# Kernel tuning notes

Measured on AMD Instinct MI355X. Metric: run time of the kernel, lower is better.

Reference implementation:

```python
import jax, jax.numpy as jnp
import numpy as np

B, N, E, H, AD, V, STEPS = 32, 256, 4, 512, 256, 10000, 5


def setup_inputs() -> dict:
    key = jax.random.key(0)
    ks = jax.random.split(key, 16)
    s = 0.02  # xavier-ish init scale
    return {
        "annotation": jax.random.randint(ks[0], (B, N), 0, V),
        "A": jax.random.normal(ks[1], (B, N, 2 * N * E), dtype=jnp.float32),
        "emb": jax.random.normal(ks[2], (V, AD), dtype=jnp.float32) * s,
        "W_in": jax.random.normal(ks[3], (E, H, H), dtype=jnp.float32) * s,
        "b_in": jnp.zeros((E, H), jnp.float32),
        "W_out": jax.random.normal(ks[4], (E, H, H), dtype=jnp.float32) * s,
        "b_out": jnp.zeros((E, H), jnp.float32),
        "Wr": jax.random.normal(ks[5], (3 * H, H), dtype=jnp.float32) * s,
        "br": jnp.zeros((H,), jnp.float32),
        "Wz": jax.random.normal(ks[6], (3 * H, H), dtype=jnp.float32) * s,
        "bz": jnp.zeros((H,), jnp.float32),
        "Wh": jax.random.normal(ks[7], (3 * H, H), dtype=jnp.float32) * s,
        "bh": jnp.zeros((H,), jnp.float32),
        "Wo": jax.random.normal(ks[8], (H + AD, H), dtype=jnp.float32) * s,
        "bo": jnp.zeros((H,), jnp.float32),
    }


def reference(annotation, A, emb, W_in, b_in, W_out, b_out,
              Wr, br, Wz, bz, Wh, bh, Wo, bo):
    ann = emb[annotation]                                   # [B, N, AD]
    pad = jnp.zeros((B, N, H - AD), ann.dtype)
    prop = jnp.concatenate([ann, pad], axis=2)              # [B, N, H]
    A_in, A_out = A[:, :, :N * E], A[:, :, N * E:]          # [B, N, N*E] each

    for _ in range(STEPS):
        # fused per-edge-type linears: [B, E, N, H] -> [B, E*N, H]
        ins = (jnp.einsum('bnd,edh->benh', prop, W_in)
               + b_in[None, :, None, :]).reshape(B, E * N, H)
        outs = (jnp.einsum('bnd,edh->benh', prop, W_out)
                + b_out[None, :, None, :]).reshape(B, E * N, H)
        a_in = jnp.matmul(A_in, ins)                        # [B, N, H]
        a_out = jnp.matmul(A_out, outs)                     # [B, N, H]
        a = jnp.concatenate([a_in, a_out, prop], axis=2)    # [B, N, 3H]
        r = jax.nn.sigmoid(a @ Wr + br)
        z = jax.nn.sigmoid(a @ Wz + bz)
        j = jnp.concatenate([a_in, a_out, r * prop], axis=2)
        h_hat = jnp.tanh(j @ Wh + bh)
        prop = (1.0 - z) * prop + z * h_hat

    join = jnp.concatenate([prop, ann], axis=2)             # [B, N, H+AD]
    return jnp.tanh(join @ Wo + bo)                         # [B, N, H]
```

## Files before the change

kernel.cpp:

```cpp
#include <hip/hip_runtime.h>
#include <hip/hip_bf16.h>
#include <cstdint>
#include <cstddef>

typedef unsigned short u16;
typedef _Float16 f16;
typedef f16 f16x8 __attribute__((ext_vector_type(8)));
typedef float f32x4 __attribute__((ext_vector_type(4)));

static __device__ inline u16 f2h(float f) {
    f16 h = (f16)f;
    return *reinterpret_cast<u16*>(&h);
}
static __device__ inline float h2f(u16 u) {
    f16 h = *reinterpret_cast<f16*>(&u);
    return (float)h;
}

#define GLL(g, l) __builtin_amdgcn_global_load_lds(                    \
    (const __attribute__((address_space(1))) void*)(g),                \
    (__attribute__((address_space(3))) void*)(l), 16, 0, 0)

static __device__ inline int xcd_swz(int fid, int nwg) {
    const int q = nwg >> 3;
    return (fid & 7) * q + (fid >> 3);
}

static __device__ inline void stage_tile(const u16* __restrict__ src, int ld,
                                         u16* lds, int wave, int lane) {
    const int r = lane >> 2;
    const int c = (lane & 3) << 3;
    const u16* g0 = src + (size_t)(wave * 32 + r) * ld + c;
    GLL(g0, lds + wave * 1024);
    GLL(g0 + (size_t)16 * ld, lds + wave * 1024 + 512);
}

static __device__ inline void compute32(const u16* lA, const u16* lB,
                                        int wq_r, int wq_c, int lr, int lk,
                                        f32x4 acc[4][4]) {
    f16x8 a[4], b[4];
    #pragma unroll
    for (int i = 0; i < 4; ++i)
        a[i] = *reinterpret_cast<const f16x8*>(&lA[(wq_r + i * 16 + lr) * 32 + lk]);
    #pragma unroll
    for (int j = 0; j < 4; ++j)
        b[j] = *reinterpret_cast<const f16x8*>(&lB[(wq_c + j * 16 + lr) * 32 + lk]);
    #pragma unroll
    for (int i = 0; i < 4; ++i)
        #pragma unroll
        for (int j = 0; j < 4; ++j)
            acc[i][j] = __builtin_amdgcn_mfma_f32_16x16x32_f16(a[i], b[j], acc[i][j], 0, 0, 0);
}

static __device__ inline void gemm128(const u16* __restrict__ a1, int lda1, int ka1,
                                      const u16* __restrict__ a2, int lda2,
                                      const u16* __restrict__ bt, int ldb,
                                      int K, int m0, int n0,
                                      u16* sA, u16* sB, f32x4 acc[4][4])
{
    const int t = threadIdx.x, lane = t & 63, wave = t >> 6;
    const int lr = lane & 15, lk = (lane >> 4) << 3;
    const int wq_r = (wave >> 1) << 6, wq_c = (wave & 1) << 6;
    const int nt = K >> 5;
    stage_tile(a1 + (size_t)m0 * lda1, lda1, sA, wave, lane);
    stage_tile(bt + (size_t)n0 * ldb, ldb, sB, wave, lane);
    __syncthreads();
    int buf = 0;
    for (int ti = 0; ti < nt; ++ti) {
        const int k1 = (ti + 1) << 5;
        if (k1 < K) {
            const u16* s;
            int ld;
            if (k1 < ka1) { s = a1 + (size_t)m0 * lda1 + k1;        ld = lda1; }
            else          { s = a2 + (size_t)m0 * lda2 + (k1 - ka1); ld = lda2; }
            stage_tile(s, ld, sA + (buf ^ 1) * 4096, wave, lane);
            stage_tile(bt + (size_t)n0 * ldb + k1, ldb, sB + (buf ^ 1) * 4096, wave, lane);
        }
        compute32(sA + buf * 4096, sB + buf * 4096, wq_r, wq_c, lr, lk, acc);
        __syncthreads();
        buf ^= 1;
    }
}

#define EPI                                         \
    const int lane = threadIdx.x & 63;              \
    const int wave = threadIdx.x >> 6;              \
    const int wq_r = (wave >> 1) << 6;              \
    const int wq_c = (wave & 1) << 6;               \
    const int lr = lane & 15;                       \
    const int l4 = (lane >> 4) << 2;

#define TDIR (32ull * 512 * 1024)

__global__ __launch_bounds__(256, 4) void k_proj(const u16* __restrict__ P,
                                                 const u16* __restrict__ Wio,
                                                 const float* __restrict__ b_in,
                                                 const float* __restrict__ b_out,
                                                 u16* __restrict__ T)
{
    __shared__ u16 sA[2 * 4096], sB[2 * 4096];
    const int fid = xcd_swz(blockIdx.x, gridDim.x);
    const int n = fid & 31, m = fid >> 5;
    const int m0 = m << 7, n0 = n << 7;
    f32x4 acc[4][4] = {};
    gemm128(P, 512, 512, P, 512, Wio, 512, 512, m0, n0, sA, sB, acc);
    EPI
    #pragma unroll
    for (int i = 0; i < 4; ++i) {
        const int row = m0 + wq_r + i * 16 + l4;
        const int b = row >> 8, mm = row & 255;
        #pragma unroll
        for (int j = 0; j < 4; ++j) {
            const int col = n0 + wq_c + j * 16 + lr;
            const int dir = col >> 11, eh = col & 2047;
            const float bia = (dir ? b_out : b_in)[eh];
            const int e = eh >> 9, h = eh & 511;
            ushort4 w4;
            w4.x = f2h(acc[i][j][0] + bia);
            w4.y = f2h(acc[i][j][1] + bia);
            w4.z = f2h(acc[i][j][2] + bia);
            w4.w = f2h(acc[i][j][3] + bia);
            u16* dst = T + (size_t)dir * TDIR + (size_t)b * 512 * 1024 + (size_t)h * 1024 + e * 256 + mm;
            *reinterpret_cast<ushort4*>(dst) = w4;
        }
    }
}

__global__ __launch_bounds__(256, 4) void k_amat(const u16* __restrict__ A16,
                                                 const u16* __restrict__ T,
                                                 u16* __restrict__ acat)
{
    __shared__ u16 sA[2 * 4096], sB[2 * 4096];
    const int fid = xcd_swz(blockIdx.x, gridDim.x);
    const int n = fid & 3, m = (fid >> 2) & 1, bd = fid >> 3;
    const int b = bd >> 1, dir = bd & 1;
    const int m0 = m << 7, n0 = n << 7;
    const u16* A1 = A16 + (size_t)b * 256 * 2048 + dir * 1024;
    const u16* Bt = T + (size_t)dir * TDIR + (size_t)b * 512 * 1024;
    f32x4 acc[4][4] = {};
    gemm128(A1, 2048, 1024, A1, 2048, Bt, 1024, 1024, m0, n0, sA, sB, acc);
    EPI
    #pragma unroll
    for (int i = 0; i < 4; ++i) {
        const int row = m0 + wq_r + i * 16 + l4;
        #pragma unroll
        for (int j = 0; j < 4; ++j) {
            const int col = n0 + wq_c + j * 16 + lr;
            #pragma unroll
            for (int v = 0; v < 4; ++v)
                acat[((size_t)b * 256 + row + v) * 1024 + dir * 512 + col] = f2h(acc[i][j][v]);
        }
    }
}

__global__ __launch_bounds__(256, 4) void k_gates(const u16* __restrict__ acat,
                                                  const u16* __restrict__ P,
                                                  const u16* __restrict__ Wrzh,
                                                  const float* __restrict__ br,
                                                  const float* __restrict__ bz,
                                                  u16* __restrict__ rp,
                                                  float* __restrict__ z,
                                                  float* __restrict__ hpart)
{
    __shared__ u16 sA[2 * 4096], sB[2 * 4096];
    const int fid = xcd_swz(blockIdx.x, gridDim.x);
    const int n = fid % 12, m = fid / 12;
    const int m0 = m << 7, n0 = n << 7;
    f32x4 acc[4][4] = {};
    gemm128(acat, 1024, 1024, P, 512, Wrzh, 1536, 1536, m0, n0, sA, sB, acc);
    EPI
    #pragma unroll
    for (int i = 0; i < 4; ++i) {
        const int row = m0 + wq_r + i * 16 + l4;
        #pragma unroll
        for (int j = 0; j < 4; ++j) {
            const int col = n0 + wq_c + j * 16 + lr;
            if (col < 512) {
                const float bia = br[col];
                #pragma unroll
                for (int v = 0; v < 4; ++v) {
                    const float s = 1.0f / (1.0f + __expf(-(acc[i][j][v] + bia)));
                    const size_t idx = (size_t)(row + v) * 512 + col;
                    rp[idx] = f2h(s * h2f(P[idx]));
                }
            } else if (col < 1024) {
                const float bia = bz[col - 512];
                #pragma unroll
                for (int v = 0; v < 4; ++v)
                    z[(size_t)(row + v) * 512 + (col - 512)] =
                        1.0f / (1.0f + __expf(-(acc[i][j][v] + bia)));
            } else {
                #pragma unroll
                for (int v = 0; v < 4; ++v)
                    hpart[(size_t)(row + v) * 512 + (col - 1024)] = acc[i][j][v];
            }
        }
    }
}

__global__ __launch_bounds__(256, 4) void k_hup(const u16* __restrict__ rp,
                                                const u16* __restrict__ WhP,
                                                const float* __restrict__ bh,
                                                const float* __restrict__ z,
                                                const float* __restrict__ hpart,
                                                u16* __restrict__ P)
{
    __shared__ u16 sA[2 * 4096], sB[2 * 4096];
    const int fid = xcd_swz(blockIdx.x, gridDim.x);
    const int n = fid & 3, m = fid >> 2;
    const int m0 = m << 7, n0 = n << 7;
    f32x4 acc[4][4] = {};
    gemm128(rp, 512, 512, rp, 512, WhP, 512, 512, m0, n0, sA, sB, acc);
    EPI
    #pragma unroll
    for (int i = 0; i < 4; ++i) {
        const int row = m0 + wq_r + i * 16 + l4;
        #pragma unroll
        for (int j = 0; j < 4; ++j) {
            const int col = n0 + wq_c + j * 16 + lr;
            const float bia = bh[col];
            #pragma unroll
            for (int v = 0; v < 4; ++v) {
                const size_t idx = (size_t)(row + v) * 512 + col;
                const float hh = tanhf(hpart[idx] + acc[i][j][v] + bia);
                const float zz = z[idx];
                const float pn = (1.0f - zz) * h2f(P[idx]) + zz * hh;
                P[idx] = f2h(pn);
            }
        }
    }
}

__global__ __launch_bounds__(256, 4) void k_final(const u16* __restrict__ P,
                                                  const u16* __restrict__ annf,
                                                  const u16* __restrict__ Wj,
                                                  const float* __restrict__ bo,
                                                  float* __restrict__ out)
{
    __shared__ u16 sA[2 * 4096], sB[2 * 4096];
    const int fid = xcd_swz(blockIdx.x, gridDim.x);
    const int n = fid & 3, m = fid >> 2;
    const int m0 = m << 7, n0 = n << 7;
    f32x4 acc[4][4] = {};
    gemm128(P, 512, 512, annf, 256, Wj, 768, 768, m0, n0, sA, sB, acc);
    EPI
    #pragma unroll
    for (int i = 0; i < 4; ++i) {
        const int row = m0 + wq_r + i * 16 + l4;
        #pragma unroll
        for (int j = 0; j < 4; ++j) {
            const int col = n0 + wq_c + j * 16 + lr;
            const float bia = bo[col];
            #pragma unroll
            for (int v = 0; v < 4; ++v)
                out[(size_t)(row + v) * 512 + col] = tanhf(acc[i][j][v] + bia);
        }
    }
}

__global__ void s_gather(const int* __restrict__ ann, const float* __restrict__ emb,
                         u16* __restrict__ P, u16* __restrict__ annf)
{
    const int gid = blockIdx.x * 256 + threadIdx.x;
    const int row = gid >> 9, d = gid & 511;
    float v = 0.0f;
    if (d < 256) v = emb[(size_t)ann[row] * 256 + d];
    const u16 h = f2h(v);
    P[gid] = h;
    if (d < 256) annf[((size_t)row << 8) + d] = h;
}

__global__ void s_cvtA(const float* __restrict__ src, u16* __restrict__ dst)
{
    const size_t base = ((size_t)blockIdx.x * 256 + threadIdx.x) * 8;
    float4 f0 = *reinterpret_cast<const float4*>(src + base);
    float4 f1 = *reinterpret_cast<const float4*>(src + base + 4);
    ushort4 p0 = { f2h(f0.x), f2h(f0.y), f2h(f0.z), f2h(f0.w) };
    ushort4 p1 = { f2h(f1.x), f2h(f1.y), f2h(f1.z), f2h(f1.w) };
    *reinterpret_cast<ushort4*>(dst + base)     = p0;
    *reinterpret_cast<ushort4*>(dst + base + 4) = p1;
}

__global__ void s_wio(const float* __restrict__ Wi, const float* __restrict__ Wo,
                      u16* __restrict__ dst)
{
    const int gid = blockIdx.x * 256 + threadIdx.x;
    if (gid >= 4096 * 512) return;
    const int nn = gid >> 9, k = gid & 511;
    const int dir = nn >> 11, e = (nn >> 9) & 3, h = nn & 511;
    const float* W = dir ? Wo : Wi;
    dst[gid] = f2h(W[(size_t)e * 512 * 512 + (size_t)k * 512 + h]);
}

__global__ void s_wrzh(const float* __restrict__ Wr, const float* __restrict__ Wz,
                       const float* __restrict__ Wh, u16* __restrict__ dst)
{
    const int gid = blockIdx.x * 256 + threadIdx.x;
    if (gid >= 1536 * 1536) return;
    const int nn = gid / 1536, k = gid - nn * 1536;
    float v;
    if (nn < 512)       v = Wr[(size_t)k * 512 + nn];
    else if (nn < 1024) v = Wz[(size_t)k * 512 + (nn - 512)];
    else                v = (k < 1024) ? Wh[(size_t)k * 512 + (nn - 1024)] : 0.0f;
    dst[gid] = f2h(v);
}

__global__ void s_whp(const float* __restrict__ Wh, u16* __restrict__ dst)
{
    const int gid = blockIdx.x * 256 + threadIdx.x;
    if (gid >= 512 * 512) return;
    const int nn = gid >> 9, k = gid & 511;
    dst[gid] = f2h(Wh[(size_t)(1024 + k) * 512 + nn]);
}

__global__ void s_wj(const float* __restrict__ Wo, u16* __restrict__ dst)
{
    const int gid = blockIdx.x * 256 + threadIdx.x;
    if (gid >= 512 * 768) return;
    const int nn = gid / 768, k = gid - nn * 768;
    dst[gid] = f2h(Wo[(size_t)k * 512 + nn]);
}

extern "C" void kernel_launch(void* const* d_in, const int* in_sizes, int n_in,
                              void* d_out, int out_size, void* d_ws, size_t ws_size,
                              hipStream_t stream) {
    const int*   ann   = (const int*)d_in[0];
    const float* A     = (const float*)d_in[1];
    const float* emb   = (const float*)d_in[2];
    const float* W_in  = (const float*)d_in[3];
    const float* b_in  = (const float*)d_in[4];
    const float* W_out = (const float*)d_in[5];
    const float* b_out = (const float*)d_in[6];
    const float* Wr    = (const float*)d_in[7];
    const float* br    = (const float*)d_in[8];
    const float* Wz    = (const float*)d_in[9];
    const float* bz    = (const float*)d_in[10];
    const float* Wh    = (const float*)d_in[11];
    const float* bh    = (const float*)d_in[12];
    const float* Wo    = (const float*)d_in[13];
    const float* bo    = (const float*)d_in[14];
    float* out = (float*)d_out;

    char* ws = (char*)d_ws;
    size_t off = 0;
    auto alloc = [&](size_t bytes) -> void* {
        void* p = ws + off;
        off = (off + bytes + 255) & ~(size_t)255;
        return p;
    };
    float* z_f32 = (float*)alloc(8192ull * 512 * 4);
    float* hpart = (float*)alloc(8192ull * 512 * 4);
    u16* P     = (u16*)alloc(8192ull * 512 * 2);
    u16* rp    = (u16*)alloc(8192ull * 512 * 2);
    u16* annf  = (u16*)alloc(8192ull * 256 * 2);
    u16* acat  = (u16*)alloc(8192ull * 1024 * 2);
    u16* A16   = (u16*)alloc(8192ull * 2048 * 2);
    u16* T     = (u16*)alloc(2 * TDIR * 2);
    u16* WioT  = (u16*)alloc(4096ull * 512 * 2);
    u16* WrzhT = (u16*)alloc(1536ull * 1536 * 2);
    u16* WhPT  = (u16*)alloc(512ull * 512 * 2);
    u16* WjT   = (u16*)alloc(512ull * 768 * 2);

    s_gather<<<16384, 256, 0, stream>>>(ann, emb, P, annf);
    s_cvtA<<<8192, 256, 0, stream>>>(A, A16);
    s_wio<<<(4096 * 512 + 255) / 256, 256, 0, stream>>>(W_in, W_out, WioT);
    s_wrzh<<<(1536 * 1536 + 255) / 256, 256, 0, stream>>>(Wr, Wz, Wh, WrzhT);
    s_whp<<<(512 * 512 + 255) / 256, 256, 0, stream>>>(Wh, WhPT);
    s_wj<<<(512 * 768 + 255) / 256, 256, 0, stream>>>(Wo, WjT);

    for (int s = 0; s < 5; ++s) {
        k_proj<<<2048, 256, 0, stream>>>(P, WioT, b_in, b_out, T);
        k_amat<<<512, 256, 0, stream>>>(A16, T, acat);
        k_gates<<<768, 256, 0, stream>>>(acat, P, WrzhT, br, bz, rp, z_f32, hpart);
        k_hup<<<256, 256, 0, stream>>>(rp, WhPT, bh, z_f32, hpart, P);
    }
    k_final<<<256, 256, 0, stream>>>(P, annf, WjT, bo, out);
}
```

Baseline: 965.4 us.

## Replace 128x128 GEMM tiles with 256x256 eight-wave pipelined GEMM for three kernels

Adds a gemm256 routine that uses 512-thread blocks, 256x256 output tiles and 64-wide K slices. It stages A/B halves into XOR-swizzled LDS with global_load_lds and runs a phased schedule that interleaves loads with MFMA bursts, using explicit vmcnt waits, barriers and setprio. k_proj, k_amat and k_gates move to this routine with smaller grids, which should raise data reuse per block and cut LDS bank conflicts. The cost is far fewer blocks: k_amat drops to 128 blocks, which can underfill the 256 CUs, and the hand-written wait counts are fragile.

```diff
diff --git a/kernel.cpp b/kernel.cpp
--- a/kernel.cpp
+++ b/kernel.cpp
@@ -8,11 +8,11 @@
 typedef f16 f16x8 __attribute__((ext_vector_type(8)));
 typedef float f32x4 __attribute__((ext_vector_type(4)));
 
-static __device__ inline u16 f2h(float f) {
+static __device__ __forceinline__ u16 f2h(float f) {
     f16 h = (f16)f;
     return *reinterpret_cast<u16*>(&h);
 }
-static __device__ inline float h2f(u16 u) {
+static __device__ __forceinline__ float h2f(u16 u) {
     f16 h = *reinterpret_cast<f16*>(&u);
     return (float)h;
 }
@@ -21,13 +21,237 @@
     (const __attribute__((address_space(1))) void*)(g),                \
     (__attribute__((address_space(3))) void*)(l), 16, 0, 0)
 
-static __device__ inline int xcd_swz(int fid, int nwg) {
+#define BARR() __builtin_amdgcn_s_barrier()
+#define VMCNT(n) { asm volatile("s_waitcnt vmcnt(" #n ")" ::: "memory"); \
+                   __builtin_amdgcn_sched_barrier(0); }
+
+static __device__ __forceinline__ int xcd_swz(int fid, int nwg) {
     const int q = nwg >> 3;
     return (fid & 7) * q + (fid >> 3);
 }
 
-static __device__ inline void stage_tile(const u16* __restrict__ src, int ld,
-                                         u16* lds, int wave, int lane) {
+#define TDIR (32ull * 512 * 1024)
+
+
+static __device__ __forceinline__ void stage_ht(const u16* __restrict__ src, int ld,
+                                                u16* ldsHalf, int t) {
+    #pragma unroll
+    for (int s = 0; s < 2; ++s) {
+        const int o = s * 8192 + t * 16;
+        const int row = o >> 7;
+        const int scolb = (o & 127) ^ ((row & 12) << 3);
+        GLL(src + (size_t)row * ld + (scolb >> 1),
+            ldsHalf + s * 4096 + (t >> 6) * 512);
+    }
+}
+
+template<int HH, bool BL>
+static __device__ __forceinline__ void ph_read(const u16* cA, const u16* cB,
+                                               int lr, int ce, int brb,
+                                               f16x8 a[4], f16x8 b[4]) {
+    #pragma unroll
+    for (int i = 0; i < 4; ++i)
+        a[i] = *reinterpret_cast<const f16x8*>(&cA[((HH * 4 + i) * 16 + lr) * 64 + ce]);
+    if (BL) {
+        #pragma unroll
+        for (int j = 0; j < 4; ++j)
+            b[j] = *reinterpret_cast<const f16x8*>(&cB[(brb + j * 16 + lr) * 64 + ce]);
+    }
+}
+
+template<int HH>
+static __device__ __forceinline__ void ph_mfma(const f16x8 a[4], const f16x8 b[4],
+                                               f32x4 acc[8][4]) {
+    asm volatile("s_waitcnt lgkmcnt(0)" ::: "memory");
+    __builtin_amdgcn_sched_barrier(0);
+    __builtin_amdgcn_s_setprio(1);
+    #pragma unroll
+    for (int i = 0; i < 4; ++i)
+        #pragma unroll
+        for (int j = 0; j < 4; ++j)
+            acc[HH * 4 + i][j] =
+                __builtin_amdgcn_mfma_f32_16x16x32_f16(a[i], b[j], acc[HH * 4 + i][j], 0, 0, 0);
+    __builtin_amdgcn_s_setprio(0);
+}
+
+#define PHASE(HH, CE, BL, STAGE, VMW)              \
+    { f16x8 a[4];                                  \
+      ph_read<HH, BL>(cA, cB, lr, CE, brb, a, b);  \
+      STAGE;                                       \
+      VMW                                          \
+      BARR();                                      \
+      ph_mfma<HH>(a, b, acc);                      \
+      BARR(); }
+
+static __device__ __forceinline__ void gemm256(const u16* __restrict__ a1, int lda1, int ka1,
+                                               const u16* __restrict__ a2, int lda2,
+                                               const u16* __restrict__ bt, int ldb,
+                                               int K, int m0, int n0,
+                                               u16* sA, u16* sB, f32x4 acc[8][4])
+{
+    const int t = threadIdx.x;
+    const int lane = t & 63, wave = t >> 6;
+    const int wm = wave >> 2, wn = wave & 3;
+    const int lr = lane & 15, hi8 = (lane >> 4) << 3;
+    const int brb = (wn & 1) << 6;
+    const int ce0 = hi8 ^ ((lr & 12) << 2);
+    const int ce1 = ce0 ^ 32;
+    const u16* A0 = sA + wm * 8192;
+    const u16* A1h = sA + (2 + wm) * 8192;
+    const u16* B0 = sB + (wn >> 1) * 8192;
+    const u16* B1h = sB + (2 + (wn >> 1)) * 8192;
+
+    auto stA = [&](int kt, int h) {
+        const int kcol = kt << 6;
+        const u16* p; int ld;
+        if (kcol < ka1) { p = a1 + (size_t)(m0 + (h << 7)) * lda1 + kcol;         ld = lda1; }
+        else            { p = a2 + (size_t)(m0 + (h << 7)) * lda2 + (kcol - ka1); ld = lda2; }
+        stage_ht(p, ld, sA + (((kt & 1) << 1) + h) * 8192, t);
+    };
+    auto stB = [&](int kt, int h) {
+        stage_ht(bt + (size_t)(n0 + (h << 7)) * ldb + (kt << 6), ldb,
+                 sB + (((kt & 1) << 1) + h) * 8192, t);
+    };
+
+    stA(0, 0); stA(0, 1); stB(0, 0); stB(0, 1); stB(1, 0);
+    VMCNT(2)
+    BARR();
+
+    f16x8 b[4];
+    const int NI2 = K >> 7;
+    const u16 *cA, *cB;
+    for (int j = 0; j < NI2; ++j) {
+        const int kA = 2 * j + 1, kB = 2 * j + 2, kC = 2 * j + 3;
+        cA = A0; cB = B0;
+        PHASE(0, ce0, true , stB(kA, 1), )
+        PHASE(1, ce0, false, stA(kA, 0), )
+        PHASE(0, ce1, true , stA(kA, 1), )
+        PHASE(1, ce1, false, stB(kB, 0), VMCNT(2))
+        cA = A1h; cB = B1h;
+        PHASE(0, ce0, true , stB(kB, 1), )
+        PHASE(1, ce0, false, stA(kB, 0), )
+        PHASE(0, ce1, true , stA(kB, 1), )
+        PHASE(1, ce1, false, stB(kC, 0), VMCNT(2))
+    }
+    asm volatile("s_waitcnt vmcnt(0)" ::: "memory");
+}
+
+#define EPI8                                        \
+    const int lane = threadIdx.x & 63;              \
+    const int wave = threadIdx.x >> 6;              \
+    const int wm = wave >> 2;                       \
+    const int wn = wave & 3;                        \
+    const int lr = lane & 15;                       \
+    const int l4 = (lane >> 4) << 2;
+
+__global__ __launch_bounds__(512, 2) void k_proj(const u16* __restrict__ P,
+                                                 const u16* __restrict__ Wio,
+                                                 const float* __restrict__ b_in,
+                                                 const float* __restrict__ b_out,
+                                                 u16* __restrict__ T)
+{
+    __shared__ u16 sA[4 * 8192], sB[4 * 8192];
+    const int fid = xcd_swz(blockIdx.x, gridDim.x);
+    const int n = fid & 15, m = fid >> 4;
+    const int m0 = m << 8, n0 = n << 8;
+    f32x4 acc[8][4] = {};
+    gemm256(P, 512, 512, P, 512, Wio, 512, 512, m0, n0, sA, sB, acc);
+    EPI8
+    #pragma unroll
+    for (int fm = 0; fm < 8; ++fm) {
+        const int row = m0 + (wm << 7) + fm * 16 + l4;
+        const int b = row >> 8, mm = row & 255;
+        #pragma unroll
+        for (int fn = 0; fn < 4; ++fn) {
+            const int col = n0 + (wn << 6) + fn * 16 + lr;
+            const int dir = col >> 11, eh = col & 2047;
+            const float bia = (dir ? b_out : b_in)[eh];
+            const int e = eh >> 9, hh = eh & 511;
+            ushort4 w4;
+            w4.x = f2h(acc[fm][fn][0] + bia);
+            w4.y = f2h(acc[fm][fn][1] + bia);
+            w4.z = f2h(acc[fm][fn][2] + bia);
+            w4.w = f2h(acc[fm][fn][3] + bia);
+            *reinterpret_cast<ushort4*>(&T[(size_t)dir * TDIR + (size_t)b * 512 * 1024
+                                           + (size_t)hh * 1024 + e * 256 + mm]) = w4;
+        }
+    }
+}
+
+__global__ __launch_bounds__(512, 2) void k_amat(const u16* __restrict__ A16,
+                                                 const u16* __restrict__ T,
+                                                 u16* __restrict__ acat)
+{
+    __shared__ u16 sA[4 * 8192], sB[4 * 8192];
+    const int fid = xcd_swz(blockIdx.x, gridDim.x);
+    const int n = fid & 1, bd = fid >> 1;
+    const int b = bd >> 1, dir = bd & 1;
+    const int n0 = n << 8;
+    const u16* A1 = A16 + (size_t)b * 256 * 2048 + dir * 1024;
+    const u16* Bt = T + (size_t)dir * TDIR + (size_t)b * 512 * 1024;
+    f32x4 acc[8][4] = {};
+    gemm256(A1, 2048, 1024, A1, 2048, Bt, 1024, 1024, 0, n0, sA, sB, acc);
+    EPI8
+    #pragma unroll
+    for (int fm = 0; fm < 8; ++fm) {
+        const int row = (wm << 7) + fm * 16 + l4;
+        #pragma unroll
+        for (int fn = 0; fn < 4; ++fn) {
+            const int col = n0 + (wn << 6) + fn * 16 + lr;
+            #pragma unroll
+            for (int v = 0; v < 4; ++v)
+                acat[((size_t)b * 256 + row + v) * 1024 + dir * 512 + col] = f2h(acc[fm][fn][v]);
+        }
+    }
+}
+
+__global__ __launch_bounds__(512, 2) void k_gates(const u16* __restrict__ acat,
+                                                  const u16* __restrict__ P,
+                                                  const u16* __restrict__ Wrzh,
+                                                  const float* __restrict__ br,
+                                                  const float* __restrict__ bz,
+                                                  u16* __restrict__ rp,
+                                                  float* __restrict__ z,
+                                                  float* __restrict__ hpart)
+{
+    __shared__ u16 sA[4 * 8192], sB[4 * 8192];
+    const int fid = xcd_swz(blockIdx.x, gridDim.x);
+    const int n = fid % 6, m = fid / 6;
+    const int m0 = m << 8, n0 = n << 8;
+    f32x4 acc[8][4] = {};
+    gemm256(acat, 1024, 1024, P, 512, Wrzh, 1536, 1536, m0, n0, sA, sB, acc);
+    EPI8
+    #pragma unroll
+    for (int fm = 0; fm < 8; ++fm) {
+        const int row = m0 + (wm << 7) + fm * 16 + l4;
+        #pragma unroll
+        for (int fn = 0; fn < 4; ++fn) {
+            const int col = n0 + (wn << 6) + fn * 16 + lr;
+            if (n0 < 512) {
+                const float bia = br[col];
+                #pragma unroll
+                for (int v = 0; v < 4; ++v) {
+                    const float s = 1.0f / (1.0f + __expf(-(acc[fm][fn][v] + bia)));
+                    const size_t idx = (size_t)(row + v) * 512 + col;
+                    rp[idx] = f2h(s * h2f(P[idx]));
+                }
+            } else if (n0 < 1024) {
+                const float bia = bz[col - 512];
+                #pragma unroll
+                for (int v = 0; v < 4; ++v)
+                    z[(size_t)(row + v) * 512 + (col - 512)] =
+                        1.0f / (1.0f + __expf(-(acc[fm][fn][v] + bia)));
+            } else {
+                #pragma unroll
+                for (int v = 0; v < 4; ++v)
+                    hpart[(size_t)(row + v) * 512 + (col - 1024)] = acc[fm][fn][v];
+            }
+        }
+    }
+}
+
+static __device__ __forceinline__ void stage_tile(const u16* __restrict__ src, int ld,
+                                                  u16* lds, int wave, int lane) {
     const int r = lane >> 2;
     const int c = (lane & 3) << 3;
     const u16* g0 = src + (size_t)(wave * 32 + r) * ld + c;
@@ -35,9 +259,9 @@
     GLL(g0 + (size_t)16 * ld, lds + wave * 1024 + 512);
 }
 
-static __device__ inline void compute32(const u16* lA, const u16* lB,
-                                        int wq_r, int wq_c, int lr, int lk,
-                                        f32x4 acc[4][4]) {
+static __device__ __forceinline__ void compute32(const u16* lA, const u16* lB,
+                                                 int wq_r, int wq_c, int lr, int lk,
+                                                 f32x4 acc[4][4]) {
     f16x8 a[4], b[4];
     #pragma unroll
     for (int i = 0; i < 4; ++i)
@@ -52,11 +276,11 @@
             acc[i][j] = __builtin_amdgcn_mfma_f32_16x16x32_f16(a[i], b[j], acc[i][j], 0, 0, 0);
 }
 
-static __device__ inline void gemm128(const u16* __restrict__ a1, int lda1, int ka1,
-                                      const u16* __restrict__ a2, int lda2,
-                                      const u16* __restrict__ bt, int ldb,
-                                      int K, int m0, int n0,
-                                      u16* sA, u16* sB, f32x4 acc[4][4])
+static __device__ __forceinline__ void gemm128(const u16* __restrict__ a1, int lda1, int ka1,
+                                               const u16* __restrict__ a2, int lda2,
+                                               const u16* __restrict__ bt, int ldb,
+                                               int K, int m0, int n0,
+                                               u16* sA, u16* sB, f32x4 acc[4][4])
 {
     const int t = threadIdx.x, lane = t & 63, wave = t >> 6;
     const int lr = lane & 15, lk = (lane >> 4) << 3;
@@ -71,7 +295,7 @@
         if (k1 < K) {
             const u16* s;
             int ld;
-            if (k1 < ka1) { s = a1 + (size_t)m0 * lda1 + k1;        ld = lda1; }
+            if (k1 < ka1) { s = a1 + (size_t)m0 * lda1 + k1;         ld = lda1; }
             else          { s = a2 + (size_t)m0 * lda2 + (k1 - ka1); ld = lda2; }
             stage_tile(s, ld, sA + (buf ^ 1) * 4096, wave, lane);
             stage_tile(bt + (size_t)n0 * ldb + k1, ldb, sB + (buf ^ 1) * 4096, wave, lane);
@@ -89,114 +313,6 @@
     const int wq_c = (wave & 1) << 6;               \
     const int lr = lane & 15;                       \
     const int l4 = (lane >> 4) << 2;
-
-#define TDIR (32ull * 512 * 1024)
-
-__global__ __launch_bounds__(256, 4) void k_proj(const u16* __restrict__ P,
-                                                 const u16* __restrict__ Wio,
-                                                 const float* __restrict__ b_in,
-                                                 const float* __restrict__ b_out,
-                                                 u16* __restrict__ T)
-{
-    __shared__ u16 sA[2 * 4096], sB[2 * 4096];
-    const int fid = xcd_swz(blockIdx.x, gridDim.x);
-    const int n = fid & 31, m = fid >> 5;
-    const int m0 = m << 7, n0 = n << 7;
-    f32x4 acc[4][4] = {};
-    gemm128(P, 512, 512, P, 512, Wio, 512, 512, m0, n0, sA, sB, acc);
-    EPI
-    #pragma unroll
-    for (int i = 0; i < 4; ++i) {
-        const int row = m0 + wq_r + i * 16 + l4;
-        const int b = row >> 8, mm = row & 255;
-        #pragma unroll
-        for (int j = 0; j < 4; ++j) {
-            const int col = n0 + wq_c + j * 16 + lr;
-            const int dir = col >> 11, eh = col & 2047;
-            const float bia = (dir ? b_out : b_in)[eh];
-            const int e = eh >> 9, h = eh & 511;
-            ushort4 w4;
-            w4.x = f2h(acc[i][j][0] + bia);
-            w4.y = f2h(acc[i][j][1] + bia);
-            w4.z = f2h(acc[i][j][2] + bia);
-            w4.w = f2h(acc[i][j][3] + bia);
-            u16* dst = T + (size_t)dir * TDIR + (size_t)b * 512 * 1024 + (size_t)h * 1024 + e * 256 + mm;
-            *reinterpret_cast<ushort4*>(dst) = w4;
-        }
-    }
-}
-
-__global__ __launch_bounds__(256, 4) void k_amat(const u16* __restrict__ A16,
-                                                 const u16* __restrict__ T,
-                                                 u16* __restrict__ acat)
-{
-    __shared__ u16 sA[2 * 4096], sB[2 * 4096];
-    const int fid = xcd_swz(blockIdx.x, gridDim.x);
-    const int n = fid & 3, m = (fid >> 2) & 1, bd = fid >> 3;
-    const int b = bd >> 1, dir = bd & 1;
-    const int m0 = m << 7, n0 = n << 7;
-    const u16* A1 = A16 + (size_t)b * 256 * 2048 + dir * 1024;
-    const u16* Bt = T + (size_t)dir * TDIR + (size_t)b * 512 * 1024;
-    f32x4 acc[4][4] = {};
-    gemm128(A1, 2048, 1024, A1, 2048, Bt, 1024, 1024, m0, n0, sA, sB, acc);
-    EPI
-    #pragma unroll
-    for (int i = 0; i < 4; ++i) {
-        const int row = m0 + wq_r + i * 16 + l4;
-        #pragma unroll
-        for (int j = 0; j < 4; ++j) {
-            const int col = n0 + wq_c + j * 16 + lr;
-            #pragma unroll
-            for (int v = 0; v < 4; ++v)
-                acat[((size_t)b * 256 + row + v) * 1024 + dir * 512 + col] = f2h(acc[i][j][v]);
-        }
-    }
-}
-
-__global__ __launch_bounds__(256, 4) void k_gates(const u16* __restrict__ acat,
-                                                  const u16* __restrict__ P,
-                                                  const u16* __restrict__ Wrzh,
-                                                  const float* __restrict__ br,
-                                                  const float* __restrict__ bz,
-                                                  u16* __restrict__ rp,
-                                                  float* __restrict__ z,
-                                                  float* __restrict__ hpart)
-{
-    __shared__ u16 sA[2 * 4096], sB[2 * 4096];
-    const int fid = xcd_swz(blockIdx.x, gridDim.x);
-    const int n = fid % 12, m = fid / 12;
-    const int m0 = m << 7, n0 = n << 7;
-    f32x4 acc[4][4] = {};
-    gemm128(acat, 1024, 1024, P, 512, Wrzh, 1536, 1536, m0, n0, sA, sB, acc);
-    EPI
-    #pragma unroll
-    for (int i = 0; i < 4; ++i) {
-        const int row = m0 + wq_r + i * 16 + l4;
-        #pragma unroll
-        for (int j = 0; j < 4; ++j) {
-            const int col = n0 + wq_c + j * 16 + lr;
-            if (col < 512) {
-                const float bia = br[col];
-                #pragma unroll
-                for (int v = 0; v < 4; ++v) {
-                    const float s = 1.0f / (1.0f + __expf(-(acc[i][j][v] + bia)));
-                    const size_t idx = (size_t)(row + v) * 512 + col;
-                    rp[idx] = f2h(s * h2f(P[idx]));
-                }
-            } else if (col < 1024) {
-                const float bia = bz[col - 512];
-                #pragma unroll
-                for (int v = 0; v < 4; ++v)
-                    z[(size_t)(row + v) * 512 + (col - 512)] =
-                        1.0f / (1.0f + __expf(-(acc[i][j][v] + bia)));
-            } else {
-                #pragma unroll
-                for (int v = 0; v < 4; ++v)
-                    hpart[(size_t)(row + v) * 512 + (col - 1024)] = acc[i][j][v];
-            }
-        }
-    }
-}
 
 __global__ __launch_bounds__(256, 4) void k_hup(const u16* __restrict__ rp,
                                                 const u16* __restrict__ WhP,
@@ -369,9 +485,9 @@
     s_wj<<<(512 * 768 + 255) / 256, 256, 0, stream>>>(Wo, WjT);
 
     for (int s = 0; s < 5; ++s) {
-        k_proj<<<2048, 256, 0, stream>>>(P, WioT, b_in, b_out, T);
-        k_amat<<<512, 256, 0, stream>>>(A16, T, acat);
-        k_gates<<<768, 256, 0, stream>>>(acat, P, WrzhT, br, bz, rp, z_f32, hpart);
+        k_proj<<<512, 512, 0, stream>>>(P, WioT, b_in, b_out, T);
+        k_amat<<<128, 512, 0, stream>>>(A16, T, acat);
+        k_gates<<<192, 512, 0, stream>>>(acat, P, WrzhT, br, bz, rp, z_f32, hpart);
         k_hup<<<256, 256, 0, stream>>>(rp, WhPT, bh, z_f32, hpart, P);
     }
     k_final<<<256, 256, 0, stream>>>(P, annf, WjT, bo, out);
```

After: 1.141 ms. +18.2%, slower.

## Use 128x64 GEMM tiles for small-grid kernels and store gate intermediates in fp16

Applied to the files above, without the earlier changes.

Adds a 128x64 tile GEMM variant and uses it in k_amat, k_gates and k_hup, doubling their grid sizes (512->1024, 768->1536, 256->512) to fill more CUs on the 256-CU part. The z and h-partial intermediates move from fp32 to fp16, halving their write and read traffic between k_gates and k_hup. Smaller tiles cut data reuse per block, which raises total global and LDS traffic for the B operand. fp16 storage of z and hpart adds some rounding error.

```diff
diff --git a/kernel.cpp b/kernel.cpp
--- a/kernel.cpp
+++ b/kernel.cpp
@@ -8,11 +8,11 @@
 typedef f16 f16x8 __attribute__((ext_vector_type(8)));
 typedef float f32x4 __attribute__((ext_vector_type(4)));
 
-static __device__ inline u16 f2h(float f) {
+static __device__ __forceinline__ u16 f2h(float f) {
     f16 h = (f16)f;
     return *reinterpret_cast<u16*>(&h);
 }
-static __device__ inline float h2f(u16 u) {
+static __device__ __forceinline__ float h2f(u16 u) {
     f16 h = *reinterpret_cast<f16*>(&u);
     return (float)h;
 }
@@ -21,13 +21,15 @@
     (const __attribute__((address_space(1))) void*)(g),                \
     (__attribute__((address_space(3))) void*)(l), 16, 0, 0)
 
-static __device__ inline int xcd_swz(int fid, int nwg) {
+static __device__ __forceinline__ int xcd_swz(int fid, int nwg) {
     const int q = nwg >> 3;
     return (fid & 7) * q + (fid >> 3);
 }
 
-static __device__ inline void stage_tile(const u16* __restrict__ src, int ld,
-                                         u16* lds, int wave, int lane) {
+#define TDIR (32ull * 512 * 1024)
+
+static __device__ __forceinline__ void stage_tile(const u16* __restrict__ src, int ld,
+                                                  u16* lds, int wave, int lane) {
     const int r = lane >> 2;
     const int c = (lane & 3) << 3;
     const u16* g0 = src + (size_t)(wave * 32 + r) * ld + c;
@@ -35,9 +37,14 @@
     GLL(g0 + (size_t)16 * ld, lds + wave * 1024 + 512);
 }
 
-static __device__ inline void compute32(const u16* lA, const u16* lB,
-                                        int wq_r, int wq_c, int lr, int lk,
-                                        f32x4 acc[4][4]) {
+static __device__ __forceinline__ void stage_tile64(const u16* __restrict__ src, int ld,
+                                                    u16* lds, int t) {
+    GLL(src + (size_t)(t >> 2) * ld + ((t & 3) << 3), lds + ((t >> 6) << 9));
+}
+
+static __device__ __forceinline__ void compute32(const u16* lA, const u16* lB,
+                                                 int wq_r, int wq_c, int lr, int lk,
+                                                 f32x4 acc[4][4]) {
     f16x8 a[4], b[4];
     #pragma unroll
     for (int i = 0; i < 4; ++i)
@@ -52,11 +59,11 @@
             acc[i][j] = __builtin_amdgcn_mfma_f32_16x16x32_f16(a[i], b[j], acc[i][j], 0, 0, 0);
 }
 
-static __device__ inline void gemm128(const u16* __restrict__ a1, int lda1, int ka1,
-                                      const u16* __restrict__ a2, int lda2,
-                                      const u16* __restrict__ bt, int ldb,
-                                      int K, int m0, int n0,
-                                      u16* sA, u16* sB, f32x4 acc[4][4])
+static __device__ __forceinline__ void gemm128(const u16* __restrict__ a1, int lda1, int ka1,
+                                               const u16* __restrict__ a2, int lda2,
+                                               const u16* __restrict__ bt, int ldb,
+                                               int K, int m0, int n0,
+                                               u16* sA, u16* sB, f32x4 acc[4][4])
 {
     const int t = threadIdx.x, lane = t & 63, wave = t >> 6;
     const int lr = lane & 15, lk = (lane >> 4) << 3;
@@ -71,12 +78,55 @@
         if (k1 < K) {
             const u16* s;
             int ld;
-            if (k1 < ka1) { s = a1 + (size_t)m0 * lda1 + k1;        ld = lda1; }
+            if (k1 < ka1) { s = a1 + (size_t)m0 * lda1 + k1;         ld = lda1; }
             else          { s = a2 + (size_t)m0 * lda2 + (k1 - ka1); ld = lda2; }
             stage_tile(s, ld, sA + (buf ^ 1) * 4096, wave, lane);
             stage_tile(bt + (size_t)n0 * ldb + k1, ldb, sB + (buf ^ 1) * 4096, wave, lane);
         }
         compute32(sA + buf * 4096, sB + buf * 4096, wq_r, wq_c, lr, lk, acc);
+        __syncthreads();
+        buf ^= 1;
+    }
+}
+
+static __device__ __forceinline__ void gemm12864(const u16* __restrict__ a1, int lda1, int ka1,
+                                                 const u16* __restrict__ a2, int lda2,
+                                                 const u16* __restrict__ bt, int ldb,
+                                                 int K, int m0, int n0,
+                                                 u16* sA, u16* sB, f32x4 acc[2][4])
+{
+    const int t = threadIdx.x, lane = t & 63, wave = t >> 6;
+    const int lr = lane & 15, lk = (lane >> 4) << 3;
+    const int wq_r = wave << 5;
+    const int nt = K >> 5;
+    stage_tile(a1 + (size_t)m0 * lda1, lda1, sA, wave, lane);
+    stage_tile64(bt + (size_t)n0 * ldb, ldb, sB, t);
+    __syncthreads();
+    int buf = 0;
+    for (int ti = 0; ti < nt; ++ti) {
+        const int k1 = (ti + 1) << 5;
+        if (k1 < K) {
+            const u16* s;
+            int ld;
+            if (k1 < ka1) { s = a1 + (size_t)m0 * lda1 + k1;         ld = lda1; }
+            else          { s = a2 + (size_t)m0 * lda2 + (k1 - ka1); ld = lda2; }
+            stage_tile(s, ld, sA + (buf ^ 1) * 4096, wave, lane);
+            stage_tile64(bt + (size_t)n0 * ldb + k1, ldb, sB + (buf ^ 1) * 2048, t);
+        }
+        const u16* lA = sA + buf * 4096;
+        const u16* lB = sB + buf * 2048;
+        f16x8 a[2], b[4];
+        #pragma unroll
+        for (int i = 0; i < 2; ++i)
+            a[i] = *reinterpret_cast<const f16x8*>(&lA[(wq_r + i * 16 + lr) * 32 + lk]);
+        #pragma unroll
+        for (int j = 0; j < 4; ++j)
+            b[j] = *reinterpret_cast<const f16x8*>(&lB[(j * 16 + lr) * 32 + lk]);
+        #pragma unroll
+        for (int i = 0; i < 2; ++i)
+            #pragma unroll
+            for (int j = 0; j < 4; ++j)
+                acc[i][j] = __builtin_amdgcn_mfma_f32_16x16x32_f16(a[i], b[j], acc[i][j], 0, 0, 0);
         __syncthreads();
         buf ^= 1;
     }
@@ -90,7 +140,12 @@
     const int lr = lane & 15;                       \
     const int l4 = (lane >> 4) << 2;
 
-#define TDIR (32ull * 512 * 1024)
+#define EPI64                                       \
+    const int lane = threadIdx.x & 63;              \
+    const int wave = threadIdx.x >> 6;              \
+    const int wq_r = wave << 5;                     \
+    const int lr = lane & 15;                       \
+    const int l4 = (lane >> 4) << 2;
 
 __global__ __launch_bounds__(256, 4) void k_proj(const u16* __restrict__ P,
                                                  const u16* __restrict__ Wio,
@@ -114,14 +169,14 @@
             const int col = n0 + wq_c + j * 16 + lr;
             const int dir = col >> 11, eh = col & 2047;
             const float bia = (dir ? b_out : b_in)[eh];
-            const int e = eh >> 9, h = eh & 511;
+            const int e = eh >> 9, hh = eh & 511;
             ushort4 w4;
             w4.x = f2h(acc[i][j][0] + bia);
             w4.y = f2h(acc[i][j][1] + bia);
             w4.z = f2h(acc[i][j][2] + bia);
             w4.w = f2h(acc[i][j][3] + bia);
-            u16* dst = T + (size_t)dir * TDIR + (size_t)b * 512 * 1024 + (size_t)h * 1024 + e * 256 + mm;
-            *reinterpret_cast<ushort4*>(dst) = w4;
+            *reinterpret_cast<ushort4*>(&T[(size_t)dir * TDIR + (size_t)b * 512 * 1024
+                                           + (size_t)hh * 1024 + e * 256 + mm]) = w4;
         }
     }
 }
@@ -130,22 +185,22 @@
                                                  const u16* __restrict__ T,
                                                  u16* __restrict__ acat)
 {
-    __shared__ u16 sA[2 * 4096], sB[2 * 4096];
+    __shared__ u16 sA[2 * 4096], sB[2 * 2048];
     const int fid = xcd_swz(blockIdx.x, gridDim.x);
-    const int n = fid & 3, m = (fid >> 2) & 1, bd = fid >> 3;
+    const int n = fid & 7, m = (fid >> 3) & 1, bd = fid >> 4;
     const int b = bd >> 1, dir = bd & 1;
-    const int m0 = m << 7, n0 = n << 7;
+    const int m0 = m << 7, n0 = n << 6;
     const u16* A1 = A16 + (size_t)b * 256 * 2048 + dir * 1024;
     const u16* Bt = T + (size_t)dir * TDIR + (size_t)b * 512 * 1024;
-    f32x4 acc[4][4] = {};
-    gemm128(A1, 2048, 1024, A1, 2048, Bt, 1024, 1024, m0, n0, sA, sB, acc);
-    EPI
-    #pragma unroll
-    for (int i = 0; i < 4; ++i) {
+    f32x4 acc[2][4] = {};
+    gemm12864(A1, 2048, 1024, A1, 2048, Bt, 1024, 1024, m0, n0, sA, sB, acc);
+    EPI64
+    #pragma unroll
+    for (int i = 0; i < 2; ++i) {
         const int row = m0 + wq_r + i * 16 + l4;
         #pragma unroll
         for (int j = 0; j < 4; ++j) {
-            const int col = n0 + wq_c + j * 16 + lr;
+            const int col = n0 + j * 16 + lr;
             #pragma unroll
             for (int v = 0; v < 4; ++v)
                 acat[((size_t)b * 256 + row + v) * 1024 + dir * 512 + col] = f2h(acc[i][j][v]);
@@ -159,23 +214,23 @@
                                                   const float* __restrict__ br,
                                                   const float* __restrict__ bz,
                                                   u16* __restrict__ rp,
-                                                  float* __restrict__ z,
-                                                  float* __restrict__ hpart)
-{
-    __shared__ u16 sA[2 * 4096], sB[2 * 4096];
+                                                  u16* __restrict__ z16,
+                                                  u16* __restrict__ hp16)
+{
+    __shared__ u16 sA[2 * 4096], sB[2 * 2048];
     const int fid = xcd_swz(blockIdx.x, gridDim.x);
-    const int n = fid % 12, m = fid / 12;
-    const int m0 = m << 7, n0 = n << 7;
-    f32x4 acc[4][4] = {};
-    gemm128(acat, 1024, 1024, P, 512, Wrzh, 1536, 1536, m0, n0, sA, sB, acc);
-    EPI
-    #pragma unroll
-    for (int i = 0; i < 4; ++i) {
+    const int n = fid % 24, m = fid / 24;
+    const int m0 = m << 7, n0 = n << 6;
+    f32x4 acc[2][4] = {};
+    gemm12864(acat, 1024, 1024, P, 512, Wrzh, 1536, 1536, m0, n0, sA, sB, acc);
+    EPI64
+    #pragma unroll
+    for (int i = 0; i < 2; ++i) {
         const int row = m0 + wq_r + i * 16 + l4;
         #pragma unroll
         for (int j = 0; j < 4; ++j) {
-            const int col = n0 + wq_c + j * 16 + lr;
-            if (col < 512) {
+            const int col = n0 + j * 16 + lr;
+            if (n0 < 512) {
                 const float bia = br[col];
                 #pragma unroll
                 for (int v = 0; v < 4; ++v) {
@@ -183,16 +238,16 @@
                     const size_t idx = (size_t)(row + v) * 512 + col;
                     rp[idx] = f2h(s * h2f(P[idx]));
                 }
-            } else if (col < 1024) {
+            } else if (n0 < 1024) {
                 const float bia = bz[col - 512];
                 #pragma unroll
                 for (int v = 0; v < 4; ++v)
-                    z[(size_t)(row + v) * 512 + (col - 512)] =
-                        1.0f / (1.0f + __expf(-(acc[i][j][v] + bia)));
+                    z16[(size_t)(row + v) * 512 + (col - 512)] =
+                        f2h(1.0f / (1.0f + __expf(-(acc[i][j][v] + bia))));
             } else {
                 #pragma unroll
                 for (int v = 0; v < 4; ++v)
-                    hpart[(size_t)(row + v) * 512 + (col - 1024)] = acc[i][j][v];
+                    hp16[(size_t)(row + v) * 512 + (col - 1024)] = f2h(acc[i][j][v]);
             }
         }
     }
@@ -201,29 +256,29 @@
 __global__ __launch_bounds__(256, 4) void k_hup(const u16* __restrict__ rp,
                                                 const u16* __restrict__ WhP,
                                                 const float* __restrict__ bh,
-                                                const float* __restrict__ z,
-                                                const float* __restrict__ hpart,
+                                                const u16* __restrict__ z16,
+                                                const u16* __restrict__ hp16,
                                                 u16* __restrict__ P)
 {
-    __shared__ u16 sA[2 * 4096], sB[2 * 4096];
+    __shared__ u16 sA[2 * 4096], sB[2 * 2048];
     const int fid = xcd_swz(blockIdx.x, gridDim.x);
-    const int n = fid & 3, m = fid >> 2;
-    const int m0 = m << 7, n0 = n << 7;
-    f32x4 acc[4][4] = {};
-    gemm128(rp, 512, 512, rp, 512, WhP, 512, 512, m0, n0, sA, sB, acc);
-    EPI
-    #pragma unroll
-    for (int i = 0; i < 4; ++i) {
+    const int n = fid & 7, m = fid >> 3;
+    const int m0 = m << 7, n0 = n << 6;
+    f32x4 acc[2][4] = {};
+    gemm12864(rp, 512, 512, rp, 512, WhP, 512, 512, m0, n0, sA, sB, acc);
+    EPI64
+    #pragma unroll
+    for (int i = 0; i < 2; ++i) {
         const int row = m0 + wq_r + i * 16 + l4;
         #pragma unroll
         for (int j = 0; j < 4; ++j) {
-            const int col = n0 + wq_c + j * 16 + lr;
+            const int col = n0 + j * 16 + lr;
             const float bia = bh[col];
             #pragma unroll
             for (int v = 0; v < 4; ++v) {
                 const size_t idx = (size_t)(row + v) * 512 + col;
-                const float hh = tanhf(hpart[idx] + acc[i][j][v] + bia);
-                const float zz = z[idx];
+                const float hh = tanhf(h2f(hp16[idx]) + acc[i][j][v] + bia);
+                const float zz = h2f(z16[idx]);
                 const float pn = (1.0f - zz) * h2f(P[idx]) + zz * hh;
                 P[idx] = f2h(pn);
             }
@@ -348,8 +403,8 @@
         off = (off + bytes + 255) & ~(size_t)255;
         return p;
     };
-    float* z_f32 = (float*)alloc(8192ull * 512 * 4);
-    float* hpart = (float*)alloc(8192ull * 512 * 4);
+    u16* z16   = (u16*)alloc(8192ull * 512 * 2);
+    u16* hp16  = (u16*)alloc(8192ull * 512 * 2);
     u16* P     = (u16*)alloc(8192ull * 512 * 2);
     u16* rp    = (u16*)alloc(8192ull * 512 * 2);
     u16* annf  = (u16*)alloc(8192ull * 256 * 2);
@@ -370,9 +425,9 @@
 
     for (int s = 0; s < 5; ++s) {
         k_proj<<<2048, 256, 0, stream>>>(P, WioT, b_in, b_out, T);
-        k_amat<<<512, 256, 0, stream>>>(A16, T, acat);
-        k_gates<<<768, 256, 0, stream>>>(acat, P, WrzhT, br, bz, rp, z_f32, hpart);
-        k_hup<<<256, 256, 0, stream>>>(rp, WhPT, bh, z_f32, hpart, P);
+        k_amat<<<1024, 256, 0, stream>>>(A16, T, acat);
+        k_gates<<<1536, 256, 0, stream>>>(acat, P, WrzhT, br, bz, rp, z16, hp16);
+        k_hup<<<512, 256, 0, stream>>>(rp, WhPT, bh, z16, hp16, P);
     }
     k_final<<<256, 256, 0, stream>>>(P, annf, WjT, bo, out);
 }
```

After: 1.018 ms. 1.05x slower.

## Triple-buffer GEMM staging, store gate intermediates in fp16, skip zero-pad K on first step

Applied to the files above, without the earlier changes.

Replaces the double-buffered LDS pipeline with a three-stage ring that prefetches two K-tiles ahead. It waits with explicit vmcnt counts and raw barriers instead of full __syncthreads. The z and partial-h intermediates between k_gates and k_hup are now stored in fp16 instead of fp32, halving that traffic at some precision cost. In the first step, k_proj uses K=256 because the upper half of P is the zero padding. The larger LDS footprint (48KB per block) may reduce occupancy under the 4-blocks launch bound.

```diff
diff --git a/kernel.cpp b/kernel.cpp
--- a/kernel.cpp
+++ b/kernel.cpp
@@ -8,11 +8,11 @@
 typedef f16 f16x8 __attribute__((ext_vector_type(8)));
 typedef float f32x4 __attribute__((ext_vector_type(4)));
 
-static __device__ inline u16 f2h(float f) {
+static __device__ __forceinline__ u16 f2h(float f) {
     f16 h = (f16)f;
     return *reinterpret_cast<u16*>(&h);
 }
-static __device__ inline float h2f(u16 u) {
+static __device__ __forceinline__ float h2f(u16 u) {
     f16 h = *reinterpret_cast<f16*>(&u);
     return (float)h;
 }
@@ -21,13 +21,15 @@
     (const __attribute__((address_space(1))) void*)(g),                \
     (__attribute__((address_space(3))) void*)(l), 16, 0, 0)
 
-static __device__ inline int xcd_swz(int fid, int nwg) {
+static __device__ __forceinline__ int xcd_swz(int fid, int nwg) {
     const int q = nwg >> 3;
     return (fid & 7) * q + (fid >> 3);
 }
 
-static __device__ inline void stage_tile(const u16* __restrict__ src, int ld,
-                                         u16* lds, int wave, int lane) {
+#define TDIR (32ull * 512 * 1024)
+
+static __device__ __forceinline__ void stage_tile(const u16* __restrict__ src, int ld,
+                                                  u16* lds, int wave, int lane) {
     const int r = lane >> 2;
     const int c = (lane & 3) << 3;
     const u16* g0 = src + (size_t)(wave * 32 + r) * ld + c;
@@ -35,9 +37,9 @@
     GLL(g0 + (size_t)16 * ld, lds + wave * 1024 + 512);
 }
 
-static __device__ inline void compute32(const u16* lA, const u16* lB,
-                                        int wq_r, int wq_c, int lr, int lk,
-                                        f32x4 acc[4][4]) {
+static __device__ __forceinline__ void compute32(const u16* lA, const u16* lB,
+                                                 int wq_r, int wq_c, int lr, int lk,
+                                                 f32x4 acc[4][4]) {
     f16x8 a[4], b[4];
     #pragma unroll
     for (int i = 0; i < 4; ++i)
@@ -52,33 +54,48 @@
             acc[i][j] = __builtin_amdgcn_mfma_f32_16x16x32_f16(a[i], b[j], acc[i][j], 0, 0, 0);
 }
 
-static __device__ inline void gemm128(const u16* __restrict__ a1, int lda1, int ka1,
-                                      const u16* __restrict__ a2, int lda2,
-                                      const u16* __restrict__ bt, int ldb,
-                                      int K, int m0, int n0,
-                                      u16* sA, u16* sB, f32x4 acc[4][4])
+static __device__ __forceinline__ void gemm128p(const u16* __restrict__ a1, int lda1, int ka1,
+                                                const u16* __restrict__ a2, int lda2,
+                                                const u16* __restrict__ bt, int ldb,
+                                                int K, int m0, int n0,
+                                                u16* sA, u16* sB, f32x4 acc[4][4])
 {
     const int t = threadIdx.x, lane = t & 63, wave = t >> 6;
     const int lr = lane & 15, lk = (lane >> 4) << 3;
     const int wq_r = (wave >> 1) << 6, wq_c = (wave & 1) << 6;
     const int nt = K >> 5;
-    stage_tile(a1 + (size_t)m0 * lda1, lda1, sA, wave, lane);
-    stage_tile(bt + (size_t)n0 * ldb, ldb, sB, wave, lane);
-    __syncthreads();
-    int buf = 0;
+
+    auto stA = [&](int kt, u16* dst) {
+        const int k0 = kt << 5;
+        const u16* s; int ld;
+        if (k0 < ka1) { s = a1 + (size_t)m0 * lda1 + k0;         ld = lda1; }
+        else          { s = a2 + (size_t)m0 * lda2 + (k0 - ka1); ld = lda2; }
+        stage_tile(s, ld, dst, wave, lane);
+    };
+    auto stB = [&](int kt, u16* dst) {
+        stage_tile(bt + (size_t)n0 * ldb + (kt << 5), ldb, dst, wave, lane);
+    };
+
+    stA(0, sA); stB(0, sB);
+    stA(1, sA + 4096); stB(1, sB + 4096);
+    asm volatile("s_waitcnt vmcnt(4)" ::: "memory");
+    __builtin_amdgcn_s_barrier();
+    __builtin_amdgcn_sched_barrier(0);
+
     for (int ti = 0; ti < nt; ++ti) {
-        const int k1 = (ti + 1) << 5;
-        if (k1 < K) {
-            const u16* s;
-            int ld;
-            if (k1 < ka1) { s = a1 + (size_t)m0 * lda1 + k1;        ld = lda1; }
-            else          { s = a2 + (size_t)m0 * lda2 + (k1 - ka1); ld = lda2; }
-            stage_tile(s, ld, sA + (buf ^ 1) * 4096, wave, lane);
-            stage_tile(bt + (size_t)n0 * ldb + k1, ldb, sB + (buf ^ 1) * 4096, wave, lane);
-        }
-        compute32(sA + buf * 4096, sB + buf * 4096, wq_r, wq_c, lr, lk, acc);
-        __syncthreads();
-        buf ^= 1;
+        const int cur = ti % 3;
+        if (ti + 2 < nt) {
+            const int nxt = (ti + 2) % 3;
+            stA(ti + 2, sA + nxt * 4096);
+            stB(ti + 2, sB + nxt * 4096);
+        }
+        compute32(sA + cur * 4096, sB + cur * 4096, wq_r, wq_c, lr, lk, acc);
+        if (ti + 1 < nt) {
+            if (ti + 2 < nt) { asm volatile("s_waitcnt vmcnt(4)" ::: "memory"); }
+            else             { asm volatile("s_waitcnt vmcnt(0)" ::: "memory"); }
+            __builtin_amdgcn_s_barrier();
+            __builtin_amdgcn_sched_barrier(0);
+        }
     }
 }
 
@@ -90,20 +107,18 @@
     const int lr = lane & 15;                       \
     const int l4 = (lane >> 4) << 2;
 
-#define TDIR (32ull * 512 * 1024)
-
 __global__ __launch_bounds__(256, 4) void k_proj(const u16* __restrict__ P,
                                                  const u16* __restrict__ Wio,
                                                  const float* __restrict__ b_in,
                                                  const float* __restrict__ b_out,
-                                                 u16* __restrict__ T)
-{
-    __shared__ u16 sA[2 * 4096], sB[2 * 4096];
+                                                 u16* __restrict__ T, int K)
+{
+    __shared__ u16 sA[3 * 4096], sB[3 * 4096];
     const int fid = xcd_swz(blockIdx.x, gridDim.x);
     const int n = fid & 31, m = fid >> 5;
     const int m0 = m << 7, n0 = n << 7;
     f32x4 acc[4][4] = {};
-    gemm128(P, 512, 512, P, 512, Wio, 512, 512, m0, n0, sA, sB, acc);
+    gemm128p(P, 512, 512, P, 512, Wio, 512, K, m0, n0, sA, sB, acc);
     EPI
     #pragma unroll
     for (int i = 0; i < 4; ++i) {
@@ -114,14 +129,14 @@
             const int col = n0 + wq_c + j * 16 + lr;
             const int dir = col >> 11, eh = col & 2047;
             const float bia = (dir ? b_out : b_in)[eh];
-            const int e = eh >> 9, h = eh & 511;
+            const int e = eh >> 9, hh = eh & 511;
             ushort4 w4;
             w4.x = f2h(acc[i][j][0] + bia);
             w4.y = f2h(acc[i][j][1] + bia);
             w4.z = f2h(acc[i][j][2] + bia);
             w4.w = f2h(acc[i][j][3] + bia);
-            u16* dst = T + (size_t)dir * TDIR + (size_t)b * 512 * 1024 + (size_t)h * 1024 + e * 256 + mm;
-            *reinterpret_cast<ushort4*>(dst) = w4;
+            *reinterpret_cast<ushort4*>(&T[(size_t)dir * TDIR + (size_t)b * 512 * 1024
+                                           + (size_t)hh * 1024 + e * 256 + mm]) = w4;
         }
     }
 }
@@ -130,7 +145,7 @@
                                                  const u16* __restrict__ T,
                                                  u16* __restrict__ acat)
 {
-    __shared__ u16 sA[2 * 4096], sB[2 * 4096];
+    __shared__ u16 sA[3 * 4096], sB[3 * 4096];
     const int fid = xcd_swz(blockIdx.x, gridDim.x);
     const int n = fid & 3, m = (fid >> 2) & 1, bd = fid >> 3;
     const int b = bd >> 1, dir = bd & 1;
@@ -138,7 +153,7 @@
     const u16* A1 = A16 + (size_t)b * 256 * 2048 + dir * 1024;
     const u16* Bt = T + (size_t)dir * TDIR + (size_t)b * 512 * 1024;
     f32x4 acc[4][4] = {};
-    gemm128(A1, 2048, 1024, A1, 2048, Bt, 1024, 1024, m0, n0, sA, sB, acc);
+    gemm128p(A1, 2048, 1024, A1, 2048, Bt, 1024, 1024, m0, n0, sA, sB, acc);
     EPI
     #pragma unroll
     for (int i = 0; i < 4; ++i) {
@@ -159,15 +174,15 @@
                                                   const float* __restrict__ br,
                                                   const float* __restrict__ bz,
                                                   u16* __restrict__ rp,
-                                                  float* __restrict__ z,
-                                                  float* __restrict__ hpart)
-{
-    __shared__ u16 sA[2 * 4096], sB[2 * 4096];
+                                                  u16* __restrict__ z16,
+                                                  u16* __restrict__ hp16)
+{
+    __shared__ u16 sA[3 * 4096], sB[3 * 4096];
     const int fid = xcd_swz(blockIdx.x, gridDim.x);
     const int n = fid % 12, m = fid / 12;
     const int m0 = m << 7, n0 = n << 7;
     f32x4 acc[4][4] = {};
-    gemm128(acat, 1024, 1024, P, 512, Wrzh, 1536, 1536, m0, n0, sA, sB, acc);
+    gemm128p(acat, 1024, 1024, P, 512, Wrzh, 1536, 1536, m0, n0, sA, sB, acc);
     EPI
     #pragma unroll
     for (int i = 0; i < 4; ++i) {
@@ -187,12 +202,12 @@
                 const float bia = bz[col - 512];
                 #pragma unroll
                 for (int v = 0; v < 4; ++v)
-                    z[(size_t)(row + v) * 512 + (col - 512)] =
-                        1.0f / (1.0f + __expf(-(acc[i][j][v] + bia)));
+                    z16[(size_t)(row + v) * 512 + (col - 512)] =
+                        f2h(1.0f / (1.0f + __expf(-(acc[i][j][v] + bia))));
             } else {
                 #pragma unroll
                 for (int v = 0; v < 4; ++v)
-                    hpart[(size_t)(row + v) * 512 + (col - 1024)] = acc[i][j][v];
+                    hp16[(size_t)(row + v) * 512 + (col - 1024)] = f2h(acc[i][j][v]);
             }
         }
     }
@@ -201,16 +216,16 @@
 __global__ __launch_bounds__(256, 4) void k_hup(const u16* __restrict__ rp,
                                                 const u16* __restrict__ WhP,
                                                 const float* __restrict__ bh,
-                                                const float* __restrict__ z,
-                                                const float* __restrict__ hpart,
+                                                const u16* __restrict__ z16,
+                                                const u16* __restrict__ hp16,
                                                 u16* __restrict__ P)
 {
-    __shared__ u16 sA[2 * 4096], sB[2 * 4096];
+    __shared__ u16 sA[3 * 4096], sB[3 * 4096];
     const int fid = xcd_swz(blockIdx.x, gridDim.x);
     const int n = fid & 3, m = fid >> 2;
     const int m0 = m << 7, n0 = n << 7;
     f32x4 acc[4][4] = {};
-    gemm128(rp, 512, 512, rp, 512, WhP, 512, 512, m0, n0, sA, sB, acc);
+    gemm128p(rp, 512, 512, rp, 512, WhP, 512, 512, m0, n0, sA, sB, acc);
     EPI
     #pragma unroll
     for (int i = 0; i < 4; ++i) {
@@ -222,8 +237,8 @@
             #pragma unroll
             for (int v = 0; v < 4; ++v) {
                 const size_t idx = (size_t)(row + v) * 512 + col;
-                const float hh = tanhf(hpart[idx] + acc[i][j][v] + bia);
-                const float zz = z[idx];
+                const float hh = tanhf(h2f(hp16[idx]) + acc[i][j][v] + bia);
+                const float zz = h2f(z16[idx]);
                 const float pn = (1.0f - zz) * h2f(P[idx]) + zz * hh;
                 P[idx] = f2h(pn);
             }
@@ -237,12 +252,12 @@
                                                   const float* __restrict__ bo,
                                                   float* __restrict__ out)
 {
-    __shared__ u16 sA[2 * 4096], sB[2 * 4096];
+    __shared__ u16 sA[3 * 4096], sB[3 * 4096];
     const int fid = xcd_swz(blockIdx.x, gridDim.x);
     const int n = fid & 3, m = fid >> 2;
     const int m0 = m << 7, n0 = n << 7;
     f32x4 acc[4][4] = {};
-    gemm128(P, 512, 512, annf, 256, Wj, 768, 768, m0, n0, sA, sB, acc);
+    gemm128p(P, 512, 512, annf, 256, Wj, 768, 768, m0, n0, sA, sB, acc);
     EPI
     #pragma unroll
     for (int i = 0; i < 4; ++i) {
@@ -348,8 +363,8 @@
         off = (off + bytes + 255) & ~(size_t)255;
         return p;
     };
-    float* z_f32 = (float*)alloc(8192ull * 512 * 4);
-    float* hpart = (float*)alloc(8192ull * 512 * 4);
+    u16* z16   = (u16*)alloc(8192ull * 512 * 2);
+    u16* hp16  = (u16*)alloc(8192ull * 512 * 2);
     u16* P     = (u16*)alloc(8192ull * 512 * 2);
     u16* rp    = (u16*)alloc(8192ull * 512 * 2);
     u16* annf  = (u16*)alloc(8192ull * 256 * 2);
@@ -369,10 +384,10 @@
     s_wj<<<(512 * 768 + 255) / 256, 256, 0, stream>>>(Wo, WjT);
 
     for (int s = 0; s < 5; ++s) {
-        k_proj<<<2048, 256, 0, stream>>>(P, WioT, b_in, b_out, T);
+        k_proj<<<2048, 256, 0, stream>>>(P, WioT, b_in, b_out, T, s == 0 ? 256 : 512);
         k_amat<<<512, 256, 0, stream>>>(A16, T, acat);
-        k_gates<<<768, 256, 0, stream>>>(acat, P, WrzhT, br, bz, rp, z_f32, hpart);
-        k_hup<<<256, 256, 0, stream>>>(rp, WhPT, bh, z_f32, hpart, P);
+        k_gates<<<768, 256, 0, stream>>>(acat, P, WrzhT, br, bz, rp, z16, hp16);
+        k_hup<<<256, 256, 0, stream>>>(rp, WhPT, bh, z16, hp16, P);
     }
     k_final<<<256, 256, 0, stream>>>(P, annf, WjT, bo, out);
 }
```

Result: slower. 1.049 ms (+8.7%).
